# Optimization experiments

Hardware: AMD Instinct MI355X
Metric: run time of the kernel (lower is better)

## Reference

```python
import jax, jax.numpy as jnp
import numpy as np

B, L, D_MODEL, H, D_QKV = 4, 2048, 1024, 16, 64
SCALE = float(D_MODEL) ** 0.5  # note: source scales by sqrt(d_model), not sqrt(d_qkv)


def setup_inputs() -> dict:
    key = jax.random.key(0)
    ks = jax.random.split(key, 6)
    xavier_qkv = (2.0 / (D_MODEL + D_QKV)) ** 0.5
    xavier_fc = (2.0 / (H * D_QKV + D_MODEL)) ** 0.5
    return {
        "x": jax.random.normal(ks[0], (B, L, D_MODEL), dtype=jnp.float32),
        "mask": jnp.ones((B, L), dtype=jnp.int32),
        "w_q": jax.random.normal(ks[1], (H, D_MODEL, D_QKV), dtype=jnp.float32) * xavier_qkv,
        "w_k": jax.random.normal(ks[2], (H, D_MODEL, D_QKV), dtype=jnp.float32) * xavier_qkv,
        "w_v": jax.random.normal(ks[3], (H, D_MODEL, D_QKV), dtype=jnp.float32) * xavier_qkv,
        "fc_w": jax.random.normal(ks[4], (D_MODEL, H * D_QKV), dtype=jnp.float32) * xavier_fc,
        "fc_b": jnp.zeros((D_MODEL,), dtype=jnp.float32),
    }


def reference(x, mask, w_q, w_k, w_v, fc_w, fc_b):
    # x: [B, L, M]; per-head projections via einsum, as in the source
    q = jnp.einsum('blm,hmd->blhd', x, w_q)
    k = jnp.einsum('blm,hmd->blhd', x, w_k)
    v = jnp.einsum('blm,hmd->blhd', x, w_v)
    scores = jnp.einsum('blhd,bkhd->bhlk', q, k)  # [B, H, L, L]
    m = mask[:, None, None, :]  # unsqueeze(1).unsqueeze(2)
    scores = jnp.where(m == 0, jnp.asarray(-1e9, scores.dtype), scores)
    logits = jax.nn.softmax(scores / SCALE, axis=3)
    # Faithful to source einsum 'bhlk,blhd->blhd' (k is summed out of logits only)
    out = jnp.einsum('bhlk,blhd->blhd', logits, v)
    out = out.reshape(x.shape[0], x.shape[1], H * D_QKV)
    return out @ fc_w.T + fc_b
```

## Files before the change

kernel.cpp:

```cpp
#include <hip/hip_runtime.h>
#include <hip/hip_bf16.h>


typedef __attribute__((ext_vector_type(8))) short bf16x8;
typedef __attribute__((ext_vector_type(4))) float f32x4;

__device__ __forceinline__ f32x4 mfma16(bf16x8 a, bf16x8 b, f32x4 c) {
  return __builtin_amdgcn_mfma_f32_16x16x32_bf16(a, b, c, 0, 0, 0);
}

__device__ __forceinline__ unsigned short f2b(float f) {
  unsigned int u = __builtin_bit_cast(unsigned int, f);
  return (unsigned short)((u + 0x7fffu + ((u >> 16) & 1u)) >> 16);
}

__device__ __forceinline__ bf16x8 cvt8(float4 a, float4 b) {
  bf16x8 r;
  r[0] = (short)f2b(a.x); r[1] = (short)f2b(a.y); r[2] = (short)f2b(a.z); r[3] = (short)f2b(a.w);
  r[4] = (short)f2b(b.x); r[5] = (short)f2b(b.y); r[6] = (short)f2b(b.z); r[7] = (short)f2b(b.w);
  return r;
}

__device__ __forceinline__ void gld_lds16(const void* g, void* l) {
  __builtin_amdgcn_global_load_lds((const __attribute__((address_space(1))) unsigned int*)g,
                                   (__attribute__((address_space(3))) unsigned int*)l, 16, 0, 0);
}

__global__ __launch_bounds__(256) void prep(const float* __restrict__ x,
                                            const float* __restrict__ wv,
                                            const float* __restrict__ fcw,
                                            unsigned short* __restrict__ xb,
                                            unsigned short* __restrict__ wcT) {
  __shared__ __align__(16) short As[2][64 * 64];
  __shared__ __align__(16) short Bs[2][64 * 64];

  int bid = blockIdx.x, t = threadIdx.x;
  int wid = t >> 6, lane = t & 63, l16 = lane & 15, quad = lane >> 4;

  if (bid < 256) {
    int j0 = (bid >> 4) * 64;
    int m0 = (bid & 15) * 64;
    int wr = wid >> 1, wc = wid & 1;
    int rowt = t >> 3, colb = (t & 7) * 8;

    f32x4 acc[2][2];
#pragma unroll
    for (int a = 0; a < 2; a++)
#pragma unroll
      for (int b = 0; b < 2; b++) acc[a][b] = (f32x4){0.f, 0.f, 0.f, 0.f};

    float4 ra[2][2], rb[2][2];

#define LOADH(h)                                                                     \
    {                                                                                \
      _Pragma("unroll")                                                              \
      for (int c = 0; c < 2; c++) {                                                  \
        int row = c * 32 + rowt;                                                     \
        const float* pa = fcw + (j0 + row) * 1024 + (h) * 64 + colb;                 \
        ra[c][0] = *reinterpret_cast<const float4*>(pa);                             \
        ra[c][1] = *reinterpret_cast<const float4*>(pa + 4);                         \
        const float* pb = wv + (h) * 65536 + (m0 + row) * 64 + colb;                 \
        rb[c][0] = *reinterpret_cast<const float4*>(pb);                             \
        rb[c][1] = *reinterpret_cast<const float4*>(pb + 4);                         \
      }                                                                              \
    }
#define STOREH(buf)                                                                  \
    {                                                                                \
      _Pragma("unroll")                                                              \
      for (int c = 0; c < 2; c++) {                                                  \
        int row = c * 32 + rowt;                                                     \
        int bo = row * 128 + ((colb * 2) ^ ((row & 7) << 4));                        \
        *reinterpret_cast<bf16x8*>((char*)As[buf] + bo) = cvt8(ra[c][0], ra[c][1]);  \
        *reinterpret_cast<bf16x8*>((char*)Bs[buf] + bo) = cvt8(rb[c][0], rb[c][1]);  \
      }                                                                              \
    }

    LOADH(0);
    STOREH(0);
    __syncthreads();

    for (int h = 0; h < 16; ++h) {
      int cur = h & 1;
      if (h < 15) LOADH(h + 1);

      bf16x8 af[2][2], bg[2][2];
#pragma unroll
      for (int rt = 0; rt < 2; rt++) {
        int rowf = wr * 32 + rt * 16 + l16;
        int rbase = rowf * 128, rx = (rowf & 7) << 4;
        af[rt][0] = *reinterpret_cast<const bf16x8*>((char*)As[cur] + rbase + ((quad * 16) ^ rx));
        af[rt][1] = *reinterpret_cast<const bf16x8*>((char*)As[cur] + rbase + ((64 + quad * 16) ^ rx));
      }
#pragma unroll
      for (int ct = 0; ct < 2; ct++) {
        int rowf = wc * 32 + ct * 16 + l16;
        int rbase = rowf * 128, rx = (rowf & 7) << 4;
        bg[ct][0] = *reinterpret_cast<const bf16x8*>((char*)Bs[cur] + rbase + ((quad * 16) ^ rx));
        bg[ct][1] = *reinterpret_cast<const bf16x8*>((char*)Bs[cur] + rbase + ((64 + quad * 16) ^ rx));
      }
#pragma unroll
      for (int ks = 0; ks < 2; ks++)
#pragma unroll
        for (int rt = 0; rt < 2; rt++)
#pragma unroll
          for (int ct = 0; ct < 2; ct++)
            acc[rt][ct] = mfma16(af[rt][ks], bg[ct][ks], acc[rt][ct]);

      if (h < 15) STOREH(cur ^ 1);
      __syncthreads();
    }
#undef LOADH
#undef STOREH

#pragma unroll
    for (int rt = 0; rt < 2; rt++)
#pragma unroll
      for (int ct = 0; ct < 2; ct++) {
        int jj = j0 + wr * 32 + rt * 16 + quad * 4;
        int mm = m0 + wc * 32 + ct * 16 + l16;
#pragma unroll
        for (int r = 0; r < 4; r++) wcT[(jj + r) * 1024 + mm] = f2b(acc[rt][ct][r]);
      }
  } else {
    int cb = bid - 256;
    for (int ch = cb; ch < 4096; ch += 768) {
      int idx = ch * 2048 + t * 8;
      float4 a = *reinterpret_cast<const float4*>(x + idx);
      float4 b = *reinterpret_cast<const float4*>(x + idx + 4);
      *reinterpret_cast<bf16x8*>(xb + idx) = cvt8(a, b);
    }
  }
}

__global__ __launch_bounds__(256, 4) void final_gemm(const unsigned short* __restrict__ xb,
                                                     const unsigned short* __restrict__ wcT,
                                                     const float* __restrict__ fcb,
                                                     float* __restrict__ out) {
  __shared__ __align__(16) unsigned short As[2 * 128 * 32];
  __shared__ __align__(16) unsigned short Bs[2 * 64 * 32];
  int t = threadIdx.x, wid = t >> 6, lane = t & 63, l16 = lane & 15, quad = lane >> 4;
  int wr = wid >> 1, wc = wid & 1;
  int row0 = (blockIdx.x >> 4) * 128;
  int col0 = (blockIdx.x & 15) * 64;

  int w4 = wid * 4, w2 = wid * 2;
  const unsigned short* Ap[4];
  const unsigned short* Bp[2];
#pragma unroll
  for (int j = 0; j < 4; j++) {
    int blk = w4 + j, s = blk >> 3;
    int row = (blk & 7) * 16 + (lane >> 2), kq = lane & 3;
    Ap[j] = xb + (row0 + row) * 1024 + s * 32 + kq * 8;
  }
#pragma unroll
  for (int j = 0; j < 2; j++) {
    int blk = w2 + j, s = blk >> 2;
    int row = (blk & 3) * 16 + (lane >> 2), kq = lane & 3;
    Bp[j] = wcT + (col0 + row) * 1024 + s * 32 + kq * 8;
  }

  f32x4 acc[4][2];
#pragma unroll
  for (int rt = 0; rt < 4; rt++)
#pragma unroll
    for (int ct = 0; ct < 2; ct++) acc[rt][ct] = (f32x4){0.f, 0.f, 0.f, 0.f};

  for (int k0 = 0; k0 < 1024; k0 += 64) {
    __syncthreads();
#pragma unroll
    for (int j = 0; j < 4; j++) gld_lds16(Ap[j] + k0, &As[(w4 + j) * 512 + lane * 8]);
#pragma unroll
    for (int j = 0; j < 2; j++) gld_lds16(Bp[j] + k0, &Bs[(w2 + j) * 512 + lane * 8]);
    __syncthreads();
#pragma unroll
    for (int s = 0; s < 2; s++) {
      bf16x8 af[4], bfr[2];
#pragma unroll
      for (int rt = 0; rt < 4; rt++)
        af[rt] = *reinterpret_cast<const bf16x8*>(&As[s * 4096 + (wr * 64 + rt * 16 + l16) * 32 + quad * 8]);
#pragma unroll
      for (int ct = 0; ct < 2; ct++)
        bfr[ct] = *reinterpret_cast<const bf16x8*>(&Bs[s * 2048 + (wc * 32 + ct * 16 + l16) * 32 + quad * 8]);
#pragma unroll
      for (int rt = 0; rt < 4; rt++)
#pragma unroll
        for (int ct = 0; ct < 2; ct++)
          acc[rt][ct] = mfma16(af[rt], bfr[ct], acc[rt][ct]);
    }
  }

#pragma unroll
  for (int ct = 0; ct < 2; ct++) {
    int j = col0 + wc * 32 + ct * 16 + l16;
    float bias = fcb[j];
#pragma unroll
    for (int rt = 0; rt < 4; rt++) {
      int i0 = row0 + wr * 64 + rt * 16 + quad * 4;
      f32x4 a = acc[rt][ct];
#pragma unroll
      for (int r = 0; r < 4; r++) out[(i0 + r) * 1024 + j] = a[r] + bias;
    }
  }
}

extern "C" void kernel_launch(void* const* d_in, const int* in_sizes, int n_in,
                              void* d_out, int out_size, void* d_ws, size_t ws_size,
                              hipStream_t stream) {
  const float* x   = (const float*)d_in[0];
  const float* wv  = (const float*)d_in[4];
  const float* fcw = (const float*)d_in[5];
  const float* fcb = (const float*)d_in[6];
  float* out = (float*)d_out;

  char* ws = (char*)d_ws;
  unsigned short* xb  = (unsigned short*)(ws);
  unsigned short* wcT = (unsigned short*)(ws + 16777216);

  prep<<<1024, 256, 0, stream>>>(x, wv, fcw, xb, wcT);
  final_gemm<<<1024, 256, 0, stream>>>(xb, wcT, fcb, out);
}
```

Baseline: 133.5 us.

## Triple-buffer LDS loads in final GEMM with async prefetch two tiles ahead

Replaces the load-then-sync-then-compute loop in the final GEMM, which stepped through K in chunks of 64, with a three-stage ring of K=32 LDS buffers. Direct global-to-LDS loads are issued two tiles ahead, and an explicit vmcnt wait plus a single barrier per iteration overlaps memory latency with MFMA work. The cost is more iterations, each with fewer MFMAs, and correctness that depends on hand-counted vmcnt values and scheduling barriers.

New measurement: 139.7 us. 1.05x slower.

```diff
diff --git a/kernel.cpp b/kernel.cpp
--- a/kernel.cpp
+++ b/kernel.cpp
@@ -136,27 +136,59 @@
                                                      const unsigned short* __restrict__ wcT,
                                                      const float* __restrict__ fcb,
                                                      float* __restrict__ out) {
-  __shared__ __align__(16) unsigned short As[2 * 128 * 32];
-  __shared__ __align__(16) unsigned short Bs[2 * 64 * 32];
+  __shared__ __align__(16) unsigned short As[3][128 * 32];
+  __shared__ __align__(16) unsigned short Bs[3][64 * 32];
   int t = threadIdx.x, wid = t >> 6, lane = t & 63, l16 = lane & 15, quad = lane >> 4;
   int wr = wid >> 1, wc = wid & 1;
   int row0 = (blockIdx.x >> 4) * 128;
   int col0 = (blockIdx.x & 15) * 64;
 
-  int w4 = wid * 4, w2 = wid * 2;
-  const unsigned short* Ap[4];
-  const unsigned short* Bp[2];
-#pragma unroll
-  for (int j = 0; j < 4; j++) {
-    int blk = w4 + j, s = blk >> 3;
-    int row = (blk & 7) * 16 + (lane >> 2), kq = lane & 3;
-    Ap[j] = xb + (row0 + row) * 1024 + s * 32 + kq * 8;
-  }
+  const unsigned short* Ap[2];
+  const unsigned short* Bp;
 #pragma unroll
   for (int j = 0; j < 2; j++) {
-    int blk = w2 + j, s = blk >> 2;
-    int row = (blk & 3) * 16 + (lane >> 2), kq = lane & 3;
-    Bp[j] = wcT + (col0 + row) * 1024 + s * 32 + kq * 8;
+    int blk = wid * 2 + j;
+    int row = blk * 16 + (lane >> 2), kq = lane & 3;
+    Ap[j] = xb + (row0 + row) * 1024 + kq * 8;
+  }
+  {
+    int row = wid * 16 + (lane >> 2), kq = lane & 3;
+    Bp = wcT + (col0 + row) * 1024 + kq * 8;
+  }
+
+#define STAGE(tt, buf)                                                                   \
+  {                                                                                      \
+    _Pragma("unroll")                                                                    \
+    for (int j = 0; j < 2; j++)                                                          \
+      gld_lds16(Ap[j] + (tt) * 32, &As[buf][(wid * 2 + j) * 512 + lane * 8]);            \
+    gld_lds16(Bp + (tt) * 32, &Bs[buf][wid * 512 + lane * 8]);                           \
+  }
+
+#define COMPUTE(buf)                                                                     \
+  {                                                                                      \
+    bf16x8 af[4], bfr[2];                                                                \
+    _Pragma("unroll")                                                                    \
+    for (int rt = 0; rt < 4; rt++)                                                       \
+      af[rt] = *reinterpret_cast<const bf16x8*>(                                         \
+          &As[buf][(wr * 64 + rt * 16 + l16) * 32 + quad * 8]);                          \
+    _Pragma("unroll")                                                                    \
+    for (int ct = 0; ct < 2; ct++)                                                       \
+      bfr[ct] = *reinterpret_cast<const bf16x8*>(                                        \
+          &Bs[buf][(wc * 32 + ct * 16 + l16) * 32 + quad * 8]);                          \
+    _Pragma("unroll")                                                                    \
+    for (int rt = 0; rt < 4; rt++)                                                       \
+      _Pragma("unroll")                                                                  \
+      for (int ct = 0; ct < 2; ct++)                                                     \
+        acc[rt][ct] = mfma16(af[rt], bfr[ct], acc[rt][ct]);                              \
+  }
+
+#define SYNC_WAIT(WAITSTR)                                                               \
+  {                                                                                      \
+    asm volatile(WAITSTR ::: "memory");                                                  \
+    __builtin_amdgcn_sched_barrier(0);                                                   \
+    __builtin_amdgcn_s_barrier();                                                        \
+    asm volatile("" ::: "memory");                                                       \
+    __builtin_amdgcn_sched_barrier(0);                                                   \
   }
 
   f32x4 acc[4][2];
@@ -165,29 +197,26 @@
 #pragma unroll
     for (int ct = 0; ct < 2; ct++) acc[rt][ct] = (f32x4){0.f, 0.f, 0.f, 0.f};
 
-  for (int k0 = 0; k0 < 1024; k0 += 64) {
-    __syncthreads();
-#pragma unroll
-    for (int j = 0; j < 4; j++) gld_lds16(Ap[j] + k0, &As[(w4 + j) * 512 + lane * 8]);
-#pragma unroll
-    for (int j = 0; j < 2; j++) gld_lds16(Bp[j] + k0, &Bs[(w2 + j) * 512 + lane * 8]);
-    __syncthreads();
-#pragma unroll
-    for (int s = 0; s < 2; s++) {
-      bf16x8 af[4], bfr[2];
-#pragma unroll
-      for (int rt = 0; rt < 4; rt++)
-        af[rt] = *reinterpret_cast<const bf16x8*>(&As[s * 4096 + (wr * 64 + rt * 16 + l16) * 32 + quad * 8]);
-#pragma unroll
-      for (int ct = 0; ct < 2; ct++)
-        bfr[ct] = *reinterpret_cast<const bf16x8*>(&Bs[s * 2048 + (wc * 32 + ct * 16 + l16) * 32 + quad * 8]);
-#pragma unroll
-      for (int rt = 0; rt < 4; rt++)
-#pragma unroll
-        for (int ct = 0; ct < 2; ct++)
-          acc[rt][ct] = mfma16(af[rt], bfr[ct], acc[rt][ct]);
-    }
-  }
+  STAGE(0, 0);
+  STAGE(1, 1);
+
+  int cur = 0;
+  for (int tk = 0; tk < 30; ++tk) {
+    SYNC_WAIT("s_waitcnt vmcnt(3) lgkmcnt(0)");
+    int nxt = cur + 2; if (nxt >= 3) nxt -= 3;
+    STAGE(tk + 2, nxt);
+    COMPUTE(cur);
+    cur = (cur == 2) ? 0 : cur + 1;
+  }
+  SYNC_WAIT("s_waitcnt vmcnt(3) lgkmcnt(0)");
+  COMPUTE(cur);
+  cur = (cur == 2) ? 0 : cur + 1;
+  SYNC_WAIT("s_waitcnt vmcnt(0) lgkmcnt(0)");
+  COMPUTE(cur);
+
+#undef STAGE
+#undef COMPUTE
+#undef SYNC_WAIT
 
 #pragma unroll
   for (int ct = 0; ct < 2; ct++) {
```

## Split weight-combine GEMM into 32x32 tiles across all blocks and interleave x conversion

Applied to the files above, without the earlier changes.

The prep kernel previously used 256 blocks computing 64x64 tiles of the combined fc_w·w_v weight, plus 768 separate blocks converting x to bf16. Now all 1024 blocks each compute a 32x32 tile and also convert a uniform slice of x, overlapping the x conversion loads with the first weight-tile loads. This balances work across blocks and removes the long serial tail of the heavier GEMM blocks. The trade-off is less data reuse per block, since each block loads more input per output element.

Result: no change. 135.9 us (+1.8%).

```diff
diff --git a/kernel.cpp b/kernel.cpp
--- a/kernel.cpp
+++ b/kernel.cpp
@@ -31,105 +31,74 @@
                                             const float* __restrict__ fcw,
                                             unsigned short* __restrict__ xb,
                                             unsigned short* __restrict__ wcT) {
-  __shared__ __align__(16) short As[2][64 * 64];
-  __shared__ __align__(16) short Bs[2][64 * 64];
+  __shared__ __align__(16) short As[2][32 * 64];
+  __shared__ __align__(16) short Bs[2][32 * 64];
 
   int bid = blockIdx.x, t = threadIdx.x;
   int wid = t >> 6, lane = t & 63, l16 = lane & 15, quad = lane >> 4;
 
-  if (bid < 256) {
-    int j0 = (bid >> 4) * 64;
-    int m0 = (bid & 15) * 64;
-    int wr = wid >> 1, wc = wid & 1;
-    int rowt = t >> 3, colb = (t & 7) * 8;
+  int k8 = bid & 7, a = bid >> 3;
+  int j0 = (k8 * 4 + (a & 3)) * 32;
+  int m0 = (a >> 2) * 32;
+  int fr = wid >> 1, fc = wid & 1;
+  int rowt = t >> 3, colb = (t & 7) * 8;
 
-    f32x4 acc[2][2];
-#pragma unroll
-    for (int a = 0; a < 2; a++)
-#pragma unroll
-      for (int b = 0; b < 2; b++) acc[a][b] = (f32x4){0.f, 0.f, 0.f, 0.f};
-
-    float4 ra[2][2], rb[2][2];
+  float4 ra[2], rb[2];
 
 #define LOADH(h)                                                                     \
     {                                                                                \
-      _Pragma("unroll")                                                              \
-      for (int c = 0; c < 2; c++) {                                                  \
-        int row = c * 32 + rowt;                                                     \
-        const float* pa = fcw + (j0 + row) * 1024 + (h) * 64 + colb;                 \
-        ra[c][0] = *reinterpret_cast<const float4*>(pa);                             \
-        ra[c][1] = *reinterpret_cast<const float4*>(pa + 4);                         \
-        const float* pb = wv + (h) * 65536 + (m0 + row) * 64 + colb;                 \
-        rb[c][0] = *reinterpret_cast<const float4*>(pb);                             \
-        rb[c][1] = *reinterpret_cast<const float4*>(pb + 4);                         \
-      }                                                                              \
+      const float* pa = fcw + (j0 + rowt) * 1024 + (h) * 64 + colb;                  \
+      ra[0] = *reinterpret_cast<const float4*>(pa);                                  \
+      ra[1] = *reinterpret_cast<const float4*>(pa + 4);                              \
+      const float* pb = wv + (h) * 65536 + (m0 + rowt) * 64 + colb;                  \
+      rb[0] = *reinterpret_cast<const float4*>(pb);                                  \
+      rb[1] = *reinterpret_cast<const float4*>(pb + 4);                              \
     }
 #define STOREH(buf)                                                                  \
     {                                                                                \
-      _Pragma("unroll")                                                              \
-      for (int c = 0; c < 2; c++) {                                                  \
-        int row = c * 32 + rowt;                                                     \
-        int bo = row * 128 + ((colb * 2) ^ ((row & 7) << 4));                        \
-        *reinterpret_cast<bf16x8*>((char*)As[buf] + bo) = cvt8(ra[c][0], ra[c][1]);  \
-        *reinterpret_cast<bf16x8*>((char*)Bs[buf] + bo) = cvt8(rb[c][0], rb[c][1]);  \
-      }                                                                              \
+      int bo = rowt * 128 + ((colb * 2) ^ ((rowt & 7) << 4));                        \
+      *reinterpret_cast<bf16x8*>((char*)As[buf] + bo) = cvt8(ra[0], ra[1]);          \
+      *reinterpret_cast<bf16x8*>((char*)Bs[buf] + bo) = cvt8(rb[0], rb[1]);          \
     }
 
-    LOADH(0);
-    STOREH(0);
+  LOADH(0);
+
+#pragma unroll
+  for (int i = 0; i < 4; i++) {
+    int idx = (bid * 4 + i) * 2048 + t * 8;
+    float4 ca = *reinterpret_cast<const float4*>(x + idx);
+    float4 cb = *reinterpret_cast<const float4*>(x + idx + 4);
+    *reinterpret_cast<bf16x8*>(xb + idx) = cvt8(ca, cb);
+  }
+
+  STOREH(0);
+  __syncthreads();
+
+  f32x4 acc = (f32x4){0.f, 0.f, 0.f, 0.f};
+  int rowfa = fr * 16 + l16, rxa = (rowfa & 7) << 4, rba = rowfa * 128;
+  int rowfb = fc * 16 + l16, rxb = (rowfb & 7) << 4, rbb = rowfb * 128;
+
+  for (int h = 0; h < 16; ++h) {
+    int cur = h & 1;
+    if (h < 15) LOADH(h + 1);
+
+    bf16x8 af0 = *reinterpret_cast<const bf16x8*>((char*)As[cur] + rba + ((quad * 16) ^ rxa));
+    bf16x8 af1 = *reinterpret_cast<const bf16x8*>((char*)As[cur] + rba + ((64 + quad * 16) ^ rxa));
+    bf16x8 bg0 = *reinterpret_cast<const bf16x8*>((char*)Bs[cur] + rbb + ((quad * 16) ^ rxb));
+    bf16x8 bg1 = *reinterpret_cast<const bf16x8*>((char*)Bs[cur] + rbb + ((64 + quad * 16) ^ rxb));
+    acc = mfma16(af0, bg0, acc);
+    acc = mfma16(af1, bg1, acc);
+
+    if (h < 15) STOREH(cur ^ 1);
     __syncthreads();
-
-    for (int h = 0; h < 16; ++h) {
-      int cur = h & 1;
-      if (h < 15) LOADH(h + 1);
-
-      bf16x8 af[2][2], bg[2][2];
-#pragma unroll
-      for (int rt = 0; rt < 2; rt++) {
-        int rowf = wr * 32 + rt * 16 + l16;
-        int rbase = rowf * 128, rx = (rowf & 7) << 4;
-        af[rt][0] = *reinterpret_cast<const bf16x8*>((char*)As[cur] + rbase + ((quad * 16) ^ rx));
-        af[rt][1] = *reinterpret_cast<const bf16x8*>((char*)As[cur] + rbase + ((64 + quad * 16) ^ rx));
-      }
-#pragma unroll
-      for (int ct = 0; ct < 2; ct++) {
-        int rowf = wc * 32 + ct * 16 + l16;
-        int rbase = rowf * 128, rx = (rowf & 7) << 4;
-        bg[ct][0] = *reinterpret_cast<const bf16x8*>((char*)Bs[cur] + rbase + ((quad * 16) ^ rx));
-        bg[ct][1] = *reinterpret_cast<const bf16x8*>((char*)Bs[cur] + rbase + ((64 + quad * 16) ^ rx));
-      }
-#pragma unroll
-      for (int ks = 0; ks < 2; ks++)
-#pragma unroll
-        for (int rt = 0; rt < 2; rt++)
-#pragma unroll
-          for (int ct = 0; ct < 2; ct++)
-            acc[rt][ct] = mfma16(af[rt][ks], bg[ct][ks], acc[rt][ct]);
-
-      if (h < 15) STOREH(cur ^ 1);
-      __syncthreads();
-    }
+  }
 #undef LOADH
 #undef STOREH
 
+  int jj = j0 + fr * 16 + quad * 4;
+  int mm = m0 + fc * 16 + l16;
 #pragma unroll
-    for (int rt = 0; rt < 2; rt++)
-#pragma unroll
-      for (int ct = 0; ct < 2; ct++) {
-        int jj = j0 + wr * 32 + rt * 16 + quad * 4;
-        int mm = m0 + wc * 32 + ct * 16 + l16;
-#pragma unroll
-        for (int r = 0; r < 4; r++) wcT[(jj + r) * 1024 + mm] = f2b(acc[rt][ct][r]);
-      }
-  } else {
-    int cb = bid - 256;
-    for (int ch = cb; ch < 4096; ch += 768) {
-      int idx = ch * 2048 + t * 8;
-      float4 a = *reinterpret_cast<const float4*>(x + idx);
-      float4 b = *reinterpret_cast<const float4*>(x + idx + 4);
-      *reinterpret_cast<bf16x8*>(xb + idx) = cvt8(a, b);
-    }
-  }
+  for (int r = 0; r < 4; r++) wcT[(jj + r) * 1024 + mm] = f2b(acc[r]);
 }
 
 __global__ __launch_bounds__(256, 4) void final_gemm(const unsigned short* __restrict__ xb,
```
